# Kernel optimization log

Hardware: AMD Instinct MI355X
Metric: run time of the kernel (lower is better)

## Reference

```python
import jax, jax.numpy as jnp
import numpy as np

B, T, D, H = 4, 2048, 1024, 8
HD = D // H  # head_dim = 128


def setup_inputs() -> dict:
    key = jax.random.key(0)
    ks = jax.random.split(key, 10)
    s = 1.0 / np.sqrt(D)
    return {
        "x": jax.random.normal(ks[0], (B, T, D), jnp.float32),
        "y": jax.random.normal(ks[1], (B, T, D), jnp.float32),
        "Wq": jax.random.normal(ks[2], (D, D), jnp.float32) * s,
        "bq": jnp.zeros((D,), jnp.float32),
        "Wk": jax.random.normal(ks[3], (D, D), jnp.float32) * s,
        "bk": jnp.zeros((D,), jnp.float32),
        "Wv": jax.random.normal(ks[4], (D, D), jnp.float32) * s,
        "bv": jnp.zeros((D,), jnp.float32),
        "Wo": jax.random.normal(ks[5], (D, D), jnp.float32) * s,
        "bo": jnp.zeros((D,), jnp.float32),
    }


def _heads(t):
    # [B, T, D] -> [B, H, T, HD]
    b, t_, _ = t.shape
    return t.reshape(b, t_, H, HD).transpose(0, 2, 1, 3)


def reference(x, y, Wq, bq, Wk, bk, Wv, bv, Wo, bo):
    Tq, Tk = x.shape[1], y.shape[1]
    q = _heads(x @ Wq.T + bq)  # [B,H,Tq,HD]
    k = _heads(y @ Wk.T + bk)  # [B,H,Tk,HD]
    v = _heads(y @ Wv.T + bv)  # [B,H,Tk,HD]
    scale = 1.0 / np.sqrt(HD)
    logits = jnp.einsum("bhqd,bhkd->bhqk", q, k) * scale
    # causal mask: positions k > q get -inf
    causal = jnp.triu(jnp.full((Tq, Tk), -jnp.inf, jnp.float32), k=1)
    logits = logits + causal
    attn = jax.nn.softmax(logits, axis=-1)  # [B,H,Tq,Tk]
    ctx = jnp.einsum("bhqk,bhkd->bhqd", attn, v)
    ctx = ctx.transpose(0, 2, 1, 3).reshape(x.shape[0], Tq, D)
    out = ctx @ Wo.T + bo
    return out
```

## Files before the change

kernel.cpp:

```cpp
#include <hip/hip_runtime.h>
#include <math.h>

#define TB 4
#define TT 2048
#define TD 1024
#define TH 8
#define THD 128

typedef __attribute__((ext_vector_type(8))) short short8;
typedef __attribute__((ext_vector_type(4))) short short4v;
typedef __attribute__((ext_vector_type(4))) float float4v;
typedef __attribute__((ext_vector_type(16))) float float16v;

__device__ __forceinline__ short f2bf(float f) {
    union { float f; unsigned u; } v; v.f = f;
    unsigned r = v.u + 0x7FFFu + ((v.u >> 16) & 1u);
    return (short)(r >> 16);
}

__device__ __forceinline__ float bf2f(short s) {
    union { unsigned u; float f; } v;
    v.u = ((unsigned)(unsigned short)s) << 16;
    return v.f;
}

__device__ __forceinline__ short8 cvt8(float4v a, float4v b) {
    short8 r;
    r[0] = f2bf(a[0]); r[1] = f2bf(a[1]); r[2] = f2bf(a[2]); r[3] = f2bf(a[3]);
    r[4] = f2bf(b[0]); r[5] = f2bf(b[1]); r[6] = f2bf(b[2]); r[7] = f2bf(b[3]);
    return r;
}

__device__ __forceinline__ void async16(const void* g, void* l) {
    __builtin_amdgcn_global_load_lds(
        (const __attribute__((address_space(1))) unsigned int*)g,
        (__attribute__((address_space(3))) unsigned int*)l, 16, 0, 0);
}

__global__ void cvtall(const float* __restrict__ x, const float* __restrict__ y,
                       const float* __restrict__ wq, const float* __restrict__ wk,
                       const float* __restrict__ wv, const float* __restrict__ wo,
                       short* __restrict__ xyb, short* __restrict__ wb)
{
    const size_t SZ = (size_t)TB * TT * TD;
    const size_t WSZ = (size_t)TD * TD;
    int ty = blockIdx.y;
    const float* s; short* d; size_t n;
    if (ty == 0)      { s = x;  d = xyb;      n = SZ; }
    else if (ty == 1) { s = y;  d = xyb + SZ; n = SZ; }
    else {
        s = (ty == 2) ? wq : (ty == 3) ? wk : (ty == 4) ? wv : wo;
        d = wb + (size_t)(ty - 2) * WSZ; n = WSZ;
    }
    size_t i = ((size_t)blockIdx.x * blockDim.x + threadIdx.x) * 8;
    if (i >= n) return;
    float4v v0 = *(const float4v*)(s + i);
    float4v v1 = *(const float4v*)(s + i + 4);
    *(short8*)(d + i) = cvt8(v0, v1);
}

__device__ __forceinline__ void gemm_core256(const short* __restrict__ A,
                                             const short* __restrict__ W,
                                             int m0, int n0, short* SM,
                                             float4v acc[4][4])
{
    short* As = SM;
    short* Bs = SM + 32768;
    const int tid = threadIdx.x;
    const int lane = tid & 63, wid = tid >> 6;
    const int lr = lane & 15, qd = lane >> 4, sw = lane & 7;
    const int wr = wid >> 1, wc = wid & 1;
    const int rsub = lane >> 3;
    const int gj = ((lane & 7) ^ rsub) * 8;
    const int K = TD;

    const short* aSrc[4]; int aDst[4];
    const short* bSrc[2]; int bDst[2];
#pragma unroll
    for (int p = 0; p < 4; ++p) {
        int ch = wid * 4 + p;
        aSrc[p] = A + (size_t)(m0 + ch * 8 + rsub) * K + gj;
        aDst[p] = ch * 512;
    }
#pragma unroll
    for (int p = 0; p < 2; ++p) {
        int ch = wid * 2 + p;
        bSrc[p] = W + (size_t)(n0 + ch * 8 + rsub) * K + gj;
        bDst[p] = ch * 512;
    }

#pragma unroll
    for (int mt = 0; mt < 4; ++mt)
#pragma unroll
        for (int nt = 0; nt < 4; ++nt)
            acc[mt][nt] = float4v{0.f, 0.f, 0.f, 0.f};

#pragma unroll
    for (int t = 0; t < 2; ++t) {
#pragma unroll
        for (int p = 0; p < 4; ++p)
            async16(aSrc[p] + t * 64, As + t * 16384 + aDst[p]);
#pragma unroll
        for (int p = 0; p < 2; ++p)
            async16(bSrc[p] + t * 64, Bs + t * 8192 + bDst[p]);
    }
    asm volatile("s_waitcnt vmcnt(6)" ::: "memory");
    __builtin_amdgcn_sched_barrier(0);
    __builtin_amdgcn_s_barrier();

#pragma unroll 2
    for (int it = 0; it < 16; ++it) {
        const short* Ac = As + (it & 1) * 16384;
        const short* Bc = Bs + (it & 1) * 8192;
        short* Asn = As + (it & 1) * 16384;
        short* Bsn = Bs + (it & 1) * 8192;
        const int kb2 = (it + 2) * 64;
        const bool stg = (it < 14);

        short8 af[4][2], bf[4][2];

#pragma unroll
        for (int mi = 0; mi < 4; ++mi)
#pragma unroll
            for (int ks = 0; ks < 2; ++ks)
                af[mi][ks] = *(const short8*)&Ac[(wr * 64 + mi * 16 + lr) * 64 +
                                                 (((ks * 4 + qd) ^ sw) * 8)];
#pragma unroll
        for (int ni = 0; ni < 2; ++ni)
#pragma unroll
            for (int ks = 0; ks < 2; ++ks)
                bf[ni][ks] = *(const short8*)&Bc[(wc * 64 + ni * 16 + lr) * 64 +
                                                 (((ks * 4 + qd) ^ sw) * 8)];
        __builtin_amdgcn_sched_barrier(0);
#pragma unroll
        for (int ni = 2; ni < 4; ++ni)
#pragma unroll
            for (int ks = 0; ks < 2; ++ks)
                bf[ni][ks] = *(const short8*)&Bc[(wc * 64 + ni * 16 + lr) * 64 +
                                                 (((ks * 4 + qd) ^ sw) * 8)];
        asm volatile("s_waitcnt lgkmcnt(4)" ::: "memory");
        __builtin_amdgcn_sched_barrier(0);
        __builtin_amdgcn_s_setprio(1);
#pragma unroll
        for (int mi = 0; mi < 4; ++mi)
#pragma unroll
            for (int ni = 0; ni < 2; ++ni)
#pragma unroll
                for (int ks = 0; ks < 2; ++ks)
                    acc[mi][ni] = __builtin_amdgcn_mfma_f32_16x16x32_bf16(
                        af[mi][ks], bf[ni][ks], acc[mi][ni], 0, 0, 0);
        __builtin_amdgcn_s_setprio(0);
        __builtin_amdgcn_sched_barrier(0);
        asm volatile("s_waitcnt lgkmcnt(0)" ::: "memory");
        __builtin_amdgcn_sched_barrier(0);
        __builtin_amdgcn_s_barrier();
        __builtin_amdgcn_sched_barrier(0);

        if (stg) {
#pragma unroll
            for (int p = 0; p < 4; ++p)
                async16(aSrc[p] + kb2, Asn + aDst[p]);
#pragma unroll
            for (int p = 0; p < 2; ++p)
                async16(bSrc[p] + kb2, Bsn + bDst[p]);
        }
        __builtin_amdgcn_s_setprio(1);
#pragma unroll
        for (int mi = 0; mi < 4; ++mi)
#pragma unroll
            for (int ni = 2; ni < 4; ++ni)
#pragma unroll
                for (int ks = 0; ks < 2; ++ks)
                    acc[mi][ni] = __builtin_amdgcn_mfma_f32_16x16x32_bf16(
                        af[mi][ks], bf[ni][ks], acc[mi][ni], 0, 0, 0);
        __builtin_amdgcn_s_setprio(0);
        if (stg) { asm volatile("s_waitcnt vmcnt(6)" ::: "memory"); }
        else     { asm volatile("s_waitcnt vmcnt(0)" ::: "memory"); }
        __builtin_amdgcn_sched_barrier(0);
        __builtin_amdgcn_s_barrier();
    }
}

__global__ __launch_bounds__(512, 2)
void gemm_qkv8(const short* __restrict__ xyb, const short* __restrict__ wb,
               const float* __restrict__ bq, const float* __restrict__ bk,
               const float* __restrict__ bv,
               short* __restrict__ qhp, short* __restrict__ khp,
               short* __restrict__ vtp)
{
    __shared__ __attribute__((aligned(16))) short SM[49152];
    const size_t SZ = (size_t)TB * TT * TD;
    const int bid = blockIdx.x;
    const int lin = (bid & 7) * 96 + (bid >> 3);
    const int by = lin / 24, bx = lin - by * 24;
    const int mode = bx >> 3;
    const int n0 = (bx & 7) * 128;
    const int h_ = n0 >> 7;
    const int m0 = by * 256;
    const short* A = (mode == 0) ? xyb : (xyb + SZ);
    const short* W = wb + (size_t)mode * TD * TD;
    const float* bias = (mode == 0) ? bq : (mode == 1) ? bk : bv;
    const float scale = (mode == 0)
        ? (0.08838834764831845f * 1.4426950408889634f) : 1.0f;

    float4v acc[4][4];
    gemm_core256(A, W, m0, n0, SM, acc);

    const int tid = threadIdx.x;
    const int lane = tid & 63, wid = tid >> 6;
    const int lr = lane & 15, qd = lane >> 4;
    const int wr = wid >> 1, wc = wid & 1;

#pragma unroll
    for (int nt = 0; nt < 4; ++nt) {
        int col = wc * 64 + nt * 16 + lr;
        float bi = bias[n0 + col];
#pragma unroll
        for (int mt = 0; mt < 4; ++mt)
#pragma unroll
            for (int i = 0; i < 4; ++i) {
                int row = wr * 64 + mt * 16 + qd * 4 + i;
                short v = f2bf((acc[mt][nt][i] + bi) * scale);
                if (mode < 2) SM[row * 128 + col] = v;
                else          SM[col * 264 + row] = v;
            }
    }
    __syncthreads();

    if (mode < 2) {
        short* outp = (mode == 0) ? qhp : khp;
#pragma unroll
        for (int r8 = 0; r8 < 8; ++r8) {
            int row = r8 * 32 + (tid >> 4), c = tid & 15;
            short8 v = *(const short8*)&SM[row * 128 + c * 8];
            int tg = m0 + row;
            int b_ = tg >> 11, t_ = tg & (TT - 1);
            *(short8*)&outp[(((size_t)(b_ * TH + h_)) * TT + t_) * THD + c * 8] = v;
        }
    } else {
        int b_ = m0 >> 11, t0 = m0 & (TT - 1);
#pragma unroll
        for (int r8 = 0; r8 < 8; ++r8) {
            int hd = r8 * 16 + (tid >> 5), c = tid & 31;
            short8 v = *(const short8*)&SM[hd * 264 + c * 8];
            *(short8*)&vtp[(((size_t)(b_ * TH + h_)) * THD + hd) * TT + t0 + c * 8] = v;
        }
    }
}

__global__ __launch_bounds__(512, 2)
void gemm_out8(const short* __restrict__ A, const short* __restrict__ W,
               const float* __restrict__ bias, float* __restrict__ outp)
{
    __shared__ __attribute__((aligned(16))) short SM[49152];
    const int bid = blockIdx.x;
    const int lin = (bid & 7) * 32 + (bid >> 3);
    const int by = lin >> 3, bx = lin & 7;
    const int m0 = by * 256, n0 = bx * 128;

    float4v acc[4][4];
    gemm_core256(A, W, m0, n0, SM, acc);

    const int tid = threadIdx.x;
    const int lane = tid & 63, wid = tid >> 6;
    const int lr = lane & 15, qd = lane >> 4;
    const int wr = wid >> 1, wc = wid & 1;
#pragma unroll
    for (int nt = 0; nt < 4; ++nt) {
        int col = n0 + wc * 64 + nt * 16 + lr;
        float bi = bias[col];
#pragma unroll
        for (int mt = 0; mt < 4; ++mt)
#pragma unroll
            for (int i = 0; i < 4; ++i) {
                int row = m0 + wr * 64 + mt * 16 + qd * 4 + i;
                outp[(size_t)row * TD + col] = acc[mt][nt][i] + bi;
            }
    }
}

__global__ __launch_bounds__(256, 2)
void attn_fwd(const short* __restrict__ qh, const short* __restrict__ kh,
              const short* __restrict__ vt, short* __restrict__ po,
              float* __restrict__ pl)
{
    __shared__ __attribute__((aligned(16))) short Ks[2][64 * 128];
    __shared__ __attribute__((aligned(16))) short Vs[2][128 * 64];

    const int tid = threadIdx.x;
    const int lane = tid & 63, wid = tid >> 6;
    const int l31 = lane & 31, h = lane >> 5;
    const int sw7 = l31 & 7;

    const int bi = blockIdx.x;
    const int bh = bi & 31;
    const int j  = bi >> 5;
    const size_t bho = (size_t)bh * TT * THD;

    for (int u = 0; u < 2; ++u) {
        const int qt  = u ? (15 - j) : j;
        const int kv0 = u ? (qt + 1) : 0;
        const int kv1 = u ? (2 * qt + 2) : (j + 1);

        short8 qf[8];
        {
            const short* qp = qh + bho + (size_t)(qt * 128 + wid * 32 + l31) * THD;
#pragma unroll
            for (int ks = 0; ks < 8; ++ks)
                qf[ks] = *(const short8*)(qp + ks * 16 + h * 8);
        }
        float16v o[4];
#pragma unroll
        for (int db = 0; db < 4; ++db)
#pragma unroll
            for (int r = 0; r < 16; ++r) o[db][r] = 0.f;
        float li = 0.f;

        {
            const short* kbase = kh + bho + (size_t)kv0 * 64 * THD;
            const short* vbase = vt + (size_t)bh * THD * TT + (size_t)kv0 * 64;
#pragma unroll
            for (int p = 0; p < 4; ++p) {
                int ch = wid * 4 + p;
                int kr = ch * 4 + (lane >> 4);
                int kg = (lane & 15) ^ (kr & 7);
                async16(kbase + (size_t)kr * THD + kg * 8, &Ks[0][ch * 512]);
                int vr = ch * 8 + (lane >> 3);
                int vg = (lane & 7) ^ (vr & 7);
                async16(vbase + (size_t)vr * TT + vg * 8, &Vs[0][ch * 512]);
            }
        }
        __syncthreads();

        int cur = 0;
        for (int kv = kv0; kv < kv1; ++kv) {
            if (kv + 1 < kv1) {
                const short* kbase = kh + bho + (size_t)(kv + 1) * 64 * THD;
                const short* vbase = vt + (size_t)bh * THD * TT +
                                     (size_t)(kv + 1) * 64;
#pragma unroll
                for (int p = 0; p < 4; ++p) {
                    int ch = wid * 4 + p;
                    int kr = ch * 4 + (lane >> 4);
                    int kg = (lane & 15) ^ (kr & 7);
                    async16(kbase + (size_t)kr * THD + kg * 8,
                            &Ks[cur ^ 1][ch * 512]);
                    int vr = ch * 8 + (lane >> 3);
                    int vg = (lane & 7) ^ (vr & 7);
                    async16(vbase + (size_t)vr * TT + vg * 8,
                            &Vs[cur ^ 1][ch * 512]);
                }
            }

            const short* Kc = Ks[cur];
            const short* Vc = Vs[cur];

            float16v s[2];
#pragma unroll
            for (int kb = 0; kb < 2; ++kb)
#pragma unroll
                for (int r = 0; r < 16; ++r) s[kb][r] = 0.f;
#pragma unroll
            for (int ks = 0; ks < 8; ++ks) {
                int cidx = ((ks * 2 + h) ^ sw7) * 8;
                short8 kf0 = *(const short8*)&Kc[l31 * 128 + cidx];
                short8 kf1 = *(const short8*)&Kc[(32 + l31) * 128 + cidx];
                s[0] = __builtin_amdgcn_mfma_f32_32x32x16_bf16(kf0, qf[ks], s[0], 0, 0, 0);
                s[1] = __builtin_amdgcn_mfma_f32_32x32x16_bf16(kf1, qf[ks], s[1], 0, 0, 0);
            }

            if (kv >= 2 * qt) {
                int q = qt * 128 + wid * 32 + l31;
#pragma unroll
                for (int r = 0; r < 16; ++r) {
                    int key = kv * 64 + (r & 3) + 8 * (r >> 2) + 4 * h;
                    if (key > q) s[0][r] = -1e30f;
                    if (key + 32 > q) s[1][r] = -1e30f;
                }
            }

#pragma unroll
            for (int st = 0; st < 8; ++st) {
                float e0 = exp2f(s[st >> 2][(st & 3) * 4 + 0]);
                float e1 = exp2f(s[st >> 2][(st & 3) * 4 + 1]);
                float e2 = exp2f(s[st >> 2][(st & 3) * 4 + 2]);
                float e3 = exp2f(s[st >> 2][(st & 3) * 4 + 3]);
                li += (e0 + e1) + (e2 + e3);
                short4v ap;
                ap[0] = f2bf(e0); ap[1] = f2bf(e1);
                ap[2] = f2bf(e2); ap[3] = f2bf(e3);
#pragma unroll
                for (int db = 0; db < 4; ++db) {
                    short4v vf = *(const short4v*)&Vc[(db * 32 + l31) * 64 +
                                                      ((st ^ sw7) * 8) + h * 4];
                    o[db] = __builtin_amdgcn_mfma_f32_32x32x8bf16_1k(ap, vf, o[db], 0, 0, 0);
                }
            }
            __syncthreads();
            cur ^= 1;
        }

        li += __shfl_xor(li, 32);
        const int slot = (bh * 16 + qt) * 2 + u;
        if (h == 0) pl[slot * 128 + wid * 32 + l31] = li;
        short* pop = po + (size_t)slot * 16384 + (size_t)(wid * 32) * 128 + l31;
#pragma unroll
        for (int r = 0; r < 16; ++r) {
            int ql = (r & 3) + 8 * (r >> 2) + 4 * h;
#pragma unroll
            for (int db = 0; db < 4; ++db)
                pop[(size_t)ql * 128 + db * 32] = f2bf(o[db][r]);
        }
    }
}

__global__ __launch_bounds__(256)
void combine(const short* __restrict__ po, const float* __restrict__ pl,
             short* __restrict__ ctx)
{
    const unsigned i = blockIdx.x * 256 + threadIdx.x;
    const int hdv = i & 15;
    const int q   = (i >> 4) & 127;
    const int qt  = (i >> 11) & 15;
    const int bh  = i >> 15;
    const int tile = bh * 16 + qt;
    const size_t base = (size_t)tile * 2 * 16384 + (size_t)q * 128 + hdv * 8;
    short8 a = *(const short8*)&po[base];
    short8 b = *(const short8*)&po[base + 16384];
    const float inv = 1.f / (pl[tile * 2 * 128 + q] + pl[(tile * 2 + 1) * 128 + q]);
    short8 r;
#pragma unroll
    for (int k = 0; k < 8; ++k)
        r[k] = f2bf((bf2f(a[k]) + bf2f(b[k])) * inv);
    const int b_ = bh >> 3, h_ = bh & 7, t = qt * 128 + q;
    *(short8*)&ctx[((size_t)(b_ * TT + t)) * TD + h_ * THD + hdv * 8] = r;
}

extern "C" void kernel_launch(void* const* d_in, const int* in_sizes, int n_in,
                              void* d_out, int out_size, void* d_ws, size_t ws_size,
                              hipStream_t stream) {
    (void)in_sizes; (void)n_in; (void)out_size; (void)ws_size;
    const float* x  = (const float*)d_in[0];
    const float* y  = (const float*)d_in[1];
    const float* Wq = (const float*)d_in[2];
    const float* bq = (const float*)d_in[3];
    const float* Wk = (const float*)d_in[4];
    const float* bk = (const float*)d_in[5];
    const float* Wv = (const float*)d_in[6];
    const float* bv = (const float*)d_in[7];
    const float* Wo = (const float*)d_in[8];
    const float* bo = (const float*)d_in[9];
    float* out = (float*)d_out;

    const size_t SZ = (size_t)TB * TT * TD;
    const size_t WSZ = (size_t)TD * TD;
    short* xyb = (short*)d_ws;
    short* wb  = xyb + 2 * SZ;
    short* qh  = wb + 4 * WSZ;
    short* kh  = qh + SZ;
    short* vt  = kh + SZ;
    float* pl  = (float*)(vt + SZ);
    short* po  = xyb;
    short* ctx = qh;

    hipLaunchKernelGGL(cvtall, dim3(SZ / 2048, 6), dim3(256), 0, stream,
                       x, y, Wq, Wk, Wv, Wo, xyb, wb);
    hipLaunchKernelGGL(gemm_qkv8, dim3(768), dim3(512), 0, stream,
                       xyb, wb, bq, bk, bv, qh, kh, vt);
    hipLaunchKernelGGL(attn_fwd, dim3(512), dim3(256), 0, stream, qh, kh, vt, po, pl);
    hipLaunchKernelGGL(combine, dim3(4096), dim3(256), 0, stream, po, pl, ctx);
    hipLaunchKernelGGL(gemm_out8, dim3(256), dim3(512), 0, stream,
                       ctx, wb + 3 * WSZ, bo, out);
}
```

Measured before the change: 277.0 us.

## Software-pipeline LDS fragment reads across GEMM iterations with ping-pong registers

Restructures the bf16 GEMM main loop so the next k-step's A and first-half B fragments are read from shared memory while the second half of the current step's MFMAs runs. Two register fragment sets alternate between even and odd iterations. This drops one of the two workgroup barriers per k-step, and the global-load wait becomes a full vmcnt(0) before the single barrier. The aim is to hide LDS read latency and cut barrier cost. The price is more live registers under launch_bounds(512,2), which risks spills or lower occupancy.

```diff
diff --git a/kernel.cpp b/kernel.cpp
--- a/kernel.cpp
+++ b/kernel.cpp
@@ -59,6 +59,8 @@
     *(short8*)(d + i) = cvt8(v0, v1);
 }
 
+struct Frag { short8 af[4][2]; short8 b01[2][2]; };
+
 __device__ __forceinline__ void gemm_core256(const short* __restrict__ A,
                                              const short* __restrict__ W,
                                              int m0, int n0, short* SM,
@@ -95,6 +97,72 @@
         for (int nt = 0; nt < 4; ++nt)
             acc[mt][nt] = float4v{0.f, 0.f, 0.f, 0.f};
 
+    auto rd1 = [&](const short* Ab, const short* Bb, Frag& f) {
+#pragma unroll
+        for (int mi = 0; mi < 4; ++mi)
+#pragma unroll
+            for (int ks = 0; ks < 2; ++ks)
+                f.af[mi][ks] = *(const short8*)&Ab[(wr * 64 + mi * 16 + lr) * 64 +
+                                                   (((ks * 4 + qd) ^ sw) * 8)];
+#pragma unroll
+        for (int ni = 0; ni < 2; ++ni)
+#pragma unroll
+            for (int ks = 0; ks < 2; ++ks)
+                f.b01[ni][ks] = *(const short8*)&Bb[(wc * 64 + ni * 16 + lr) * 64 +
+                                                    (((ks * 4 + qd) ^ sw) * 8)];
+    };
+
+    auto body = [&](int it, Frag& fc, Frag& fn,
+                    const short* Ab, const short* Bb,
+                    short* Asn, short* Bsn,
+                    const short* An, const short* Bn) {
+        const int kb2 = (it + 2) * 64;
+        short8 b23[2][2];
+#pragma unroll
+        for (int ni = 0; ni < 2; ++ni)
+#pragma unroll
+            for (int ks = 0; ks < 2; ++ks)
+                b23[ni][ks] = *(const short8*)&Bb[(wc * 64 + (ni + 2) * 16 + lr) * 64 +
+                                                  (((ks * 4 + qd) ^ sw) * 8)];
+        asm volatile("s_waitcnt lgkmcnt(4)" ::: "memory");
+        __builtin_amdgcn_sched_barrier(0);
+        __builtin_amdgcn_s_setprio(1);
+#pragma unroll
+        for (int mi = 0; mi < 4; ++mi)
+#pragma unroll
+            for (int ni = 0; ni < 2; ++ni)
+#pragma unroll
+                for (int ks = 0; ks < 2; ++ks)
+                    acc[mi][ni] = __builtin_amdgcn_mfma_f32_16x16x32_bf16(
+                        fc.af[mi][ks], fc.b01[ni][ks], acc[mi][ni], 0, 0, 0);
+        __builtin_amdgcn_s_setprio(0);
+        __builtin_amdgcn_sched_barrier(0);
+        asm volatile("s_waitcnt vmcnt(0) lgkmcnt(0)" ::: "memory");
+        __builtin_amdgcn_sched_barrier(0);
+        __builtin_amdgcn_s_barrier();
+        __builtin_amdgcn_sched_barrier(0);
+        if (it < 14) {
+#pragma unroll
+            for (int p = 0; p < 4; ++p)
+                async16(aSrc[p] + kb2, Asn + aDst[p]);
+#pragma unroll
+            for (int p = 0; p < 2; ++p)
+                async16(bSrc[p] + kb2, Bsn + bDst[p]);
+        }
+        if (it < 15) rd1(An, Bn, fn);
+        __builtin_amdgcn_sched_barrier(0);
+        __builtin_amdgcn_s_setprio(1);
+#pragma unroll
+        for (int mi = 0; mi < 4; ++mi)
+#pragma unroll
+            for (int ni = 0; ni < 2; ++ni)
+#pragma unroll
+                for (int ks = 0; ks < 2; ++ks)
+                    acc[mi][ni + 2] = __builtin_amdgcn_mfma_f32_16x16x32_bf16(
+                        fc.af[mi][ks], b23[ni][ks], acc[mi][ni + 2], 0, 0, 0);
+        __builtin_amdgcn_s_setprio(0);
+    };
+
 #pragma unroll
     for (int t = 0; t < 2; ++t) {
 #pragma unroll
@@ -107,77 +175,17 @@
     asm volatile("s_waitcnt vmcnt(6)" ::: "memory");
     __builtin_amdgcn_sched_barrier(0);
     __builtin_amdgcn_s_barrier();
-
-#pragma unroll 2
-    for (int it = 0; it < 16; ++it) {
-        const short* Ac = As + (it & 1) * 16384;
-        const short* Bc = Bs + (it & 1) * 8192;
-        short* Asn = As + (it & 1) * 16384;
-        short* Bsn = Bs + (it & 1) * 8192;
-        const int kb2 = (it + 2) * 64;
-        const bool stg = (it < 14);
-
-        short8 af[4][2], bf[4][2];
-
-#pragma unroll
-        for (int mi = 0; mi < 4; ++mi)
-#pragma unroll
-            for (int ks = 0; ks < 2; ++ks)
-                af[mi][ks] = *(const short8*)&Ac[(wr * 64 + mi * 16 + lr) * 64 +
-                                                 (((ks * 4 + qd) ^ sw) * 8)];
-#pragma unroll
-        for (int ni = 0; ni < 2; ++ni)
-#pragma unroll
-            for (int ks = 0; ks < 2; ++ks)
-                bf[ni][ks] = *(const short8*)&Bc[(wc * 64 + ni * 16 + lr) * 64 +
-                                                 (((ks * 4 + qd) ^ sw) * 8)];
-        __builtin_amdgcn_sched_barrier(0);
-#pragma unroll
-        for (int ni = 2; ni < 4; ++ni)
-#pragma unroll
-            for (int ks = 0; ks < 2; ++ks)
-                bf[ni][ks] = *(const short8*)&Bc[(wc * 64 + ni * 16 + lr) * 64 +
-                                                 (((ks * 4 + qd) ^ sw) * 8)];
-        asm volatile("s_waitcnt lgkmcnt(4)" ::: "memory");
-        __builtin_amdgcn_sched_barrier(0);
-        __builtin_amdgcn_s_setprio(1);
-#pragma unroll
-        for (int mi = 0; mi < 4; ++mi)
-#pragma unroll
-            for (int ni = 0; ni < 2; ++ni)
-#pragma unroll
-                for (int ks = 0; ks < 2; ++ks)
-                    acc[mi][ni] = __builtin_amdgcn_mfma_f32_16x16x32_bf16(
-                        af[mi][ks], bf[ni][ks], acc[mi][ni], 0, 0, 0);
-        __builtin_amdgcn_s_setprio(0);
-        __builtin_amdgcn_sched_barrier(0);
-        asm volatile("s_waitcnt lgkmcnt(0)" ::: "memory");
-        __builtin_amdgcn_sched_barrier(0);
-        __builtin_amdgcn_s_barrier();
-        __builtin_amdgcn_sched_barrier(0);
-
-        if (stg) {
-#pragma unroll
-            for (int p = 0; p < 4; ++p)
-                async16(aSrc[p] + kb2, Asn + aDst[p]);
-#pragma unroll
-            for (int p = 0; p < 2; ++p)
-                async16(bSrc[p] + kb2, Bsn + bDst[p]);
-        }
-        __builtin_amdgcn_s_setprio(1);
-#pragma unroll
-        for (int mi = 0; mi < 4; ++mi)
-#pragma unroll
-            for (int ni = 2; ni < 4; ++ni)
-#pragma unroll
-                for (int ks = 0; ks < 2; ++ks)
-                    acc[mi][ni] = __builtin_amdgcn_mfma_f32_16x16x32_bf16(
-                        af[mi][ks], bf[ni][ks], acc[mi][ni], 0, 0, 0);
-        __builtin_amdgcn_s_setprio(0);
-        if (stg) { asm volatile("s_waitcnt vmcnt(6)" ::: "memory"); }
-        else     { asm volatile("s_waitcnt vmcnt(0)" ::: "memory"); }
-        __builtin_amdgcn_sched_barrier(0);
-        __builtin_amdgcn_s_barrier();
+    __builtin_amdgcn_sched_barrier(0);
+
+    Frag fE, fO;
+    rd1(As, Bs, fE);
+
+#pragma unroll 1
+    for (int it = 0; it < 16; it += 2) {
+        body(it,     fE, fO, As, Bs,                 As, Bs,
+                             As + 16384, Bs + 8192);
+        body(it + 1, fO, fE, As + 16384, Bs + 8192,  As + 16384, Bs + 8192,
+                             As, Bs);
     }
 }
 
```

Result: slower. 288.0 us (+4.0%).

## Use 32x32x16 bf16 MFMA for PV with packed conversion and permlane swap

Applied to the files above, without the earlier changes.

The P·V product now uses the K=16 bf16 MFMA instead of the K=8 variant. P fragments are assembled with hardware packed bf16 conversion and v_permlane32_swap to match the operand layout, and V is read as 8-short vectors. This halves the number of MFMA issues and LDS reads for PV and replaces software rounding with a single instruction. The K-tile swizzle is widened from 8 to 16 groups to reduce LDS bank conflicts. It relies on gfx950-specific instructions and on the permlane lane-mapping being exactly right.

```diff
diff --git a/kernel.cpp b/kernel.cpp
--- a/kernel.cpp
+++ b/kernel.cpp
@@ -11,6 +11,7 @@
 typedef __attribute__((ext_vector_type(4))) short short4v;
 typedef __attribute__((ext_vector_type(4))) float float4v;
 typedef __attribute__((ext_vector_type(16))) float float16v;
+typedef __attribute__((ext_vector_type(4))) unsigned uint4v;
 
 __device__ __forceinline__ short f2bf(float f) {
     union { float f; unsigned u; } v; v.f = f;
@@ -291,6 +292,7 @@
     const int lane = tid & 63, wid = tid >> 6;
     const int l31 = lane & 31, h = lane >> 5;
     const int sw7 = l31 & 7;
+    const int sw15 = l31 & 15;
 
     const int bi = blockIdx.x;
     const int bh = bi & 31;
@@ -323,7 +325,7 @@
             for (int p = 0; p < 4; ++p) {
                 int ch = wid * 4 + p;
                 int kr = ch * 4 + (lane >> 4);
-                int kg = (lane & 15) ^ (kr & 7);
+                int kg = (lane & 15) ^ (kr & 15);
                 async16(kbase + (size_t)kr * THD + kg * 8, &Ks[0][ch * 512]);
                 int vr = ch * 8 + (lane >> 3);
                 int vg = (lane & 7) ^ (vr & 7);
@@ -342,7 +344,7 @@
                 for (int p = 0; p < 4; ++p) {
                     int ch = wid * 4 + p;
                     int kr = ch * 4 + (lane >> 4);
-                    int kg = (lane & 15) ^ (kr & 7);
+                    int kg = (lane & 15) ^ (kr & 15);
                     async16(kbase + (size_t)kr * THD + kg * 8,
                             &Ks[cur ^ 1][ch * 512]);
                     int vr = ch * 8 + (lane >> 3);
@@ -362,7 +364,7 @@
                 for (int r = 0; r < 16; ++r) s[kb][r] = 0.f;
 #pragma unroll
             for (int ks = 0; ks < 8; ++ks) {
-                int cidx = ((ks * 2 + h) ^ sw7) * 8;
+                int cidx = ((ks * 2 + h) ^ sw15) * 8;
                 short8 kf0 = *(const short8*)&Kc[l31 * 128 + cidx];
                 short8 kf1 = *(const short8*)&Kc[(32 + l31) * 128 + cidx];
                 s[0] = __builtin_amdgcn_mfma_f32_32x32x16_bf16(kf0, qf[ks], s[0], 0, 0, 0);
@@ -380,20 +382,30 @@
             }
 
 #pragma unroll
-            for (int st = 0; st < 8; ++st) {
-                float e0 = exp2f(s[st >> 2][(st & 3) * 4 + 0]);
-                float e1 = exp2f(s[st >> 2][(st & 3) * 4 + 1]);
-                float e2 = exp2f(s[st >> 2][(st & 3) * 4 + 2]);
-                float e3 = exp2f(s[st >> 2][(st & 3) * 4 + 3]);
-                li += (e0 + e1) + (e2 + e3);
-                short4v ap;
-                ap[0] = f2bf(e0); ap[1] = f2bf(e1);
-                ap[2] = f2bf(e2); ap[3] = f2bf(e3);
+            for (int t = 0; t < 4; ++t) {
+                const int rA = ((2 * t) & 3) * 4, rB = ((2 * t + 1) & 3) * 4;
+                const int kb = t >> 1;
+                float eA0 = exp2f(s[kb][rA + 0]), eA1 = exp2f(s[kb][rA + 1]);
+                float eA2 = exp2f(s[kb][rA + 2]), eA3 = exp2f(s[kb][rA + 3]);
+                float eB0 = exp2f(s[kb][rB + 0]), eB1 = exp2f(s[kb][rB + 1]);
+                float eB2 = exp2f(s[kb][rB + 2]), eB3 = exp2f(s[kb][rB + 3]);
+                li += ((eA0 + eA1) + (eA2 + eA3)) + ((eB0 + eB1) + (eB2 + eB3));
+                unsigned a0, a1, b0, b1;
+                asm("v_cvt_pk_bf16_f32 %0, %1, %2" : "=v"(a0) : "v"(eA0), "v"(eA1));
+                asm("v_cvt_pk_bf16_f32 %0, %1, %2" : "=v"(a1) : "v"(eA2), "v"(eA3));
+                asm("v_cvt_pk_bf16_f32 %0, %1, %2" : "=v"(b0) : "v"(eB0), "v"(eB1));
+                asm("v_cvt_pk_bf16_f32 %0, %1, %2" : "=v"(b1) : "v"(eB2), "v"(eB3));
+                asm("v_permlane32_swap_b32 %0, %1" : "+v"(a0), "+v"(b0));
+                asm("v_permlane32_swap_b32 %0, %1" : "+v"(a1), "+v"(b1));
+                union { uint4v u; short8 s8; } pc;
+                pc.u[0] = a0; pc.u[1] = a1; pc.u[2] = b0; pc.u[3] = b1;
+                const short8 pa = pc.s8;
 #pragma unroll
                 for (int db = 0; db < 4; ++db) {
-                    short4v vf = *(const short4v*)&Vc[(db * 32 + l31) * 64 +
-                                                      ((st ^ sw7) * 8) + h * 4];
-                    o[db] = __builtin_amdgcn_mfma_f32_32x32x8bf16_1k(ap, vf, o[db], 0, 0, 0);
+                    short8 vf = *(const short8*)&Vc[(db * 32 + l31) * 64 +
+                                                    (((2 * t + h) ^ sw7) * 8)];
+                    o[db] = __builtin_amdgcn_mfma_f32_32x32x16_bf16(
+                        pa, vf, o[db], 0, 0, 0);
                 }
             }
             __syncthreads();
```

After: 281.3 us. About the same (+1.6%).
